# Kernel optimization log

Hardware: AMD Instinct MI355X
Metric: run time of the kernel (lower is better)

The kernel has to match this reference:

```python
import jax, jax.numpy as jnp
import numpy as np

N = 50000          # nodes per side (variables == clauses here)
IN, HID, OUT = 64, 128, 128
H = 4              # attention heads (self and cross)
P = 2              # num_meta_paths
E = 640000         # edges per graph
NEG = 0.2          # leaky_relu negative slope


def _glorot(key, shape):
    fan = shape[-2] + shape[-1]
    return (jax.random.normal(key, shape) * jnp.sqrt(2.0 / fan)).astype(jnp.float32)


def _ln(x, g, b):
    mu = x.mean(-1, keepdims=True)
    v = ((x - mu) ** 2).mean(-1, keepdims=True)
    return (x - mu) / jnp.sqrt(v + 1e-5) * g + b


def _segment_softmax(s, seg, num):
    # s: [E, H]; softmax over edges sharing the same seg id
    smax = jax.ops.segment_max(s, seg, num_segments=num)
    e = jnp.exp(s - smax[seg])
    den = jax.ops.segment_sum(e, seg, num_segments=num)
    return e / (den[seg] + 1e-16)


def _agg(alpha, feats, src, dst, num):
    # out[d, h, c] = sum_{e: dst[e]=d} alpha[e,h] * feats[src[e], c]
    gathered = feats[src]  # [E, C]
    outs = [jax.ops.segment_sum(alpha[:, h:h + 1] * gathered, dst, num_segments=num)
            for h in range(alpha.shape[1])]
    return jnp.stack(outs, axis=1)  # [num, H, C]


def _hga_self(x, adj, W, att_l, att_r, bias):
    # homogeneous HGAConv with self loops, concat=False (mean over heads)
    n = x.shape[0]
    xl = x @ W.T                      # [N, C]
    al = xl @ att_l                   # [N, H]
    ar = xl @ att_r                   # [N, H]
    loops = jnp.arange(n)
    src = jnp.concatenate([adj[0], loops])
    dst = jnp.concatenate([adj[1], loops])
    score = al[dst] + ar[src]         # edge_score: a_l[adj[1]] + a_r[adj[0]]
    alpha = _segment_softmax(jax.nn.leaky_relu(score, NEG), dst, n)
    out = _agg(alpha, xl, src, dst, n).mean(axis=1)  # [N, C]
    return out + bias


def _hga_cross(xv, xc, adj, Wl, Wr, att_l, att_r, bias):
    # bipartite HGAConv: adj[1] indexes var nodes, adj[0] indexes cls nodes
    n, m = xv.shape[0], xc.shape[0]
    xl = xv @ Wl.T
    xr = xc @ Wr.T
    al = xl @ att_l
    ar = xr @ att_r
    ar_ = xl @ att_r
    al_ = xr @ att_l
    c_idx, v_idx = adj[0], adj[1]
    score = al[v_idx] + ar[c_idx]        # -> normalized per var node
    score_ = ar_[v_idx] + al_[c_idx]     # transposed direction -> per cls node
    alpha = _segment_softmax(jax.nn.leaky_relu(score, NEG), v_idx, n)
    alpha_ = _segment_softmax(jax.nn.leaky_relu(score_, NEG), c_idx, m)
    out_var = _agg(alpha, xr, c_idx, v_idx, n).mean(axis=1) + bias   # [n, OUT]
    out_cls = _agg(alpha_, xl, v_idx, c_idx, m).mean(axis=1) + bias  # [m, OUT]
    return out_var, out_cls


def setup_inputs() -> dict:
    key = jax.random.key(0)
    ks = jax.random.split(key, 32)
    d = {}
    d['x_var'] = jax.random.normal(ks[0], (N, IN), dtype=jnp.float32)
    d['x_cls'] = jax.random.normal(ks[1], (N, IN), dtype=jnp.float32)
    d['mp_var'] = jax.random.randint(ks[2], (P, 2, E), 0, N)
    d['mp_cls'] = jax.random.randint(ks[3], (P, 2, E), 0, N)
    d['adj_pos'] = jax.random.randint(ks[4], (2, E), 0, N)
    d['adj_neg'] = jax.random.randint(ks[5], (2, E), 0, N)
    d['W_var_emb'] = _glorot(ks[6], (HID, IN))
    d['W_cls_emb'] = _glorot(ks[7], (HID, IN))
    d['ln_var_g'] = jnp.ones(HID); d['ln_var_b'] = jnp.zeros(HID)
    d['ln_cls_g'] = jnp.ones(HID); d['ln_cls_b'] = jnp.zeros(HID)
    d['var_pw'] = jnp.ones(P); d['cls_pw'] = jnp.ones(P)
    d['sv_W'] = _glorot(ks[8], (P, HID, HID))
    d['sv_al'] = _glorot(ks[9], (P, HID, H))
    d['sv_ar'] = _glorot(ks[10], (P, HID, H))
    d['sv_b'] = jnp.zeros((P, HID))
    d['sc_W'] = _glorot(ks[11], (P, HID, HID))
    d['sc_al'] = _glorot(ks[12], (P, HID, H))
    d['sc_ar'] = _glorot(ks[13], (P, HID, H))
    d['sc_b'] = jnp.zeros((P, HID))
    d['cp_Wl'] = _glorot(ks[14], (OUT, HID))
    d['cp_Wr'] = _glorot(ks[15], (OUT, HID))
    d['cp_al'] = _glorot(ks[16], (OUT, H))
    d['cp_ar'] = _glorot(ks[17], (OUT, H))
    d['cp_b'] = jnp.zeros(OUT)
    d['cn_Wl'] = _glorot(ks[18], (OUT, HID))
    d['cn_Wr'] = _glorot(ks[19], (OUT, HID))
    d['cn_al'] = _glorot(ks[20], (OUT, H))
    d['cn_ar'] = _glorot(ks[21], (OUT, H))
    d['cn_b'] = jnp.zeros(OUT)
    return d


def reference(x_var, x_cls, mp_var, mp_cls, adj_pos, adj_neg,
              W_var_emb, W_cls_emb, ln_var_g, ln_var_b, ln_cls_g, ln_cls_b,
              var_pw, cls_pw, sv_W, sv_al, sv_ar, sv_b, sc_W, sc_al, sc_ar, sc_b,
              cp_Wl, cp_Wr, cp_al, cp_ar, cp_b, cn_Wl, cn_Wr, cn_al, cn_ar, cn_b):
    xv = x_var @ W_var_emb.T          # [N, HID]
    xc = x_cls @ W_cls_emb.T
    # pre-norm residual self-attention, weighted sum over meta paths
    hv = _ln(xv, ln_var_g, ln_var_b)
    hc = _ln(xc, ln_cls_g, ln_cls_b)
    av = sum(var_pw[p] * _hga_self(hv, mp_var[p], sv_W[p], sv_al[p], sv_ar[p], sv_b[p]) for p in range(P))
    ac = sum(cls_pw[p] * _hga_self(hc, mp_cls[p], sc_W[p], sc_al[p], sc_ar[p], sc_b[p]) for p in range(P))
    xv = xv + av
    xc = xc + ac
    # bipartite cross attention over positive / negative literal edges
    vpos, cpos = _hga_cross(xv, xc, adj_pos, cp_Wl, cp_Wr, cp_al, cp_ar, cp_b)
    vneg, cneg = _hga_cross(xv, xc, adj_neg, cn_Wl, cn_Wr, cn_al, cn_ar, cn_b)
    return jnp.stack([vpos + vneg, cpos + cneg])  # [2, N, OUT]
```

## Files before the change

kernel.cpp:

```cpp
#include <hip/hip_runtime.h>
#include <hip/hip_bf16.h>

#define NN 50000
#define EE 640000
#define NEG 0.2f
#define CAP 64

#define BSH 9
#define NBKT 98
#define FCAP 7168
#define CHUNKA 8192
#define PA_B 79

struct Ptr8 { const int* p[8]; };
struct MArgs { const float* w[8]; const float* al[8]; const float* ar[8]; };

struct SegArg {
    const int* starts;
    const int* counts;
    const unsigned short* srt;
    const float* adst;
    const float* asrc;
    const unsigned short* feats;
    const float* pw;
    int pwi;
    int hasLoop;
};

struct ProjArgs {
    const float* in;
    const unsigned short* Wp0; const unsigned short* Wp1;
    const float* M0; const float* M1;
    unsigned short* ob0; unsigned short* ob1;
    float4* dl0; float4* dr0; float4* dl1; float4* dr1;
};

struct EmbArgs {
    const float* x; const float* Wt; const float* g; const float* b;
    const float* pw; const float* sb; float* F; float* C;
};

typedef __attribute__((ext_vector_type(8))) short short8;
typedef __attribute__((ext_vector_type(8))) unsigned short ushort8;
typedef __attribute__((ext_vector_type(4))) float floatx4;

__device__ __forceinline__ unsigned short f2bf(float x) {
    unsigned b = __float_as_uint(x);
    b = b + 0x7fffu + ((b >> 16) & 1u);
    return (unsigned short)(b >> 16);
}

__device__ __forceinline__ float4 leakyexp4(float4 ad, float4 as) {
    float v0 = ad.x + as.x, v1 = ad.y + as.y, v2 = ad.z + as.z, v3 = ad.w + as.w;
    v0 = v0 > 0.f ? v0 : NEG * v0;
    v1 = v1 > 0.f ? v1 : NEG * v1;
    v2 = v2 > 0.f ? v2 : NEG * v2;
    v3 = v3 > 0.f ? v3 : NEG * v3;
    return make_float4(__expf(v0), __expf(v1), __expf(v2), __expf(v3));
}

__global__ void prep_all(const float* __restrict__ wev, const float* __restrict__ wec,
                         float* __restrict__ Wt, MArgs a, float* __restrict__ Mbuf,
                         unsigned short* __restrict__ Wbf)
{
    int b = blockIdx.x;
    if (b < 64) {
        int i = b * 256 + threadIdx.x;
        if (i < 8192) { Wt[i] = wev[(i & 127) * 64 + (i >> 7)]; }
        else { int j = i - 8192; Wt[i] = wec[(j & 127) * 64 + (j >> 7)]; }
        return;
    }
    if (b < 128) {
        int tid = (b - 64) * 256 + threadIdx.x;
        int w = tid >> 11;
        int idx = tid & 2047;
        int tile = idx >> 6;
        int lane = idx & 63;
        int ct = tile >> 2, kc = tile & 3;
        int n = ct * 16 + (lane & 15);
        int k0 = kc * 32 + (lane >> 4) * 8;
        const float* src = a.w[w] + n * 128 + k0;
        short8 v;
#pragma unroll
        for (int j = 0; j < 8; j++) v[j] = (short)f2bf(src[j]);
        *(short8*)&Wbf[(size_t)tid * 8] = v;
        return;
    }
    {
        int w = b - 128;
        const float* W  = a.w[w];
        const float* AL = a.al[w];
        const float* AR = a.ar[w];
        for (int e = threadIdx.x; e < 1024; e += 256) {
            int k = e >> 3, h = e & 7;
            const float* att = (h < 4) ? AL : AR;
            int hh = h & 3;
            float s = 0.f;
            for (int c = 0; c < 128; c++) s += W[c * 128 + k] * att[c * 4 + hh];
            Mbuf[w * 1024 + e] = s;
        }
    }
}

__global__ void embed_ln2(EmbArgs Ea, EmbArgs Eb, int nb)
{
    __shared__ float lx[8][64];
    __shared__ float red[2][8][2];
    int half = blockIdx.x >= nb;
    const EmbArgs E = half ? Eb : Ea;
    int blk = blockIdx.x - (half ? nb : 0);
    int c = threadIdx.x;
    int n0 = blk * 8;
    for (int t = c; t < 8 * 64; t += 128) {
        lx[t >> 6][t & 63] = E.x[(size_t)(n0 + (t >> 6)) * 64 + (t & 63)];
    }
    __syncthreads();
    float acc[8];
#pragma unroll
    for (int m = 0; m < 8; m++) acc[m] = 0.f;
    for (int k = 0; k < 64; k++) {
        float w = E.Wt[k * 128 + c];
#pragma unroll
        for (int m = 0; m < 8; m++) acc[m] += lx[m][k] * w;
    }
    int lane = c & 63, wv = c >> 6;
#pragma unroll
    for (int m = 0; m < 8; m++) {
        float s1 = acc[m], s2 = acc[m] * acc[m];
        for (int off = 32; off; off >>= 1) { s1 += __shfl_xor(s1, off); s2 += __shfl_xor(s2, off); }
        if (lane == 0) { red[wv][m][0] = s1; red[wv][m][1] = s2; }
    }
    __syncthreads();
    float biassum = E.pw[0] * E.sb[c] + E.pw[1] * E.sb[128 + c];
    float gg = E.g[c], bb = E.b[c];
#pragma unroll
    for (int m = 0; m < 8; m++) {
        float s1 = red[0][m][0] + red[1][m][0];
        float s2 = red[0][m][1] + red[1][m][1];
        float mu  = s1 * (1.f / 128.f);
        float var = s2 * (1.f / 128.f) - mu * mu;
        float inv = rsqrtf(var + 1e-5f);
        float v = acc[m];
        size_t idx = (size_t)(n0 + m) * 128 + c;
        E.F[idx] = v + biassum;
        E.C[idx] = (v - mu) * inv * gg + bb;
    }
}

__global__ __launch_bounds__(256) void mfma_proj2(ProjArgs Pa, ProjArgs Pb, int nb)
{
    __shared__ float ML[2048];

    int half = blockIdx.x >= nb;
    const ProjArgs P = half ? Pb : Pa;
    int blk = blockIdx.x - (half ? nb : 0);

    int t = threadIdx.x;
    for (int i = t; i < 2048; i += 256) ML[i] = (i < 1024) ? P.M0[i] : P.M1[i - 1024];
    __syncthreads();

    int w = t >> 6, lane = t & 63;
    int rg = w & 1, chh = w >> 1;
    int ln = lane & 15, quad = lane >> 4;
    int rbase = blk * 32 + rg * 16;
    int row = rbase + ln;
    int arow = (row < NN) ? row : (NN - 1);
    const float* MLh = &ML[chh * 1024];

    short8 afrag[4];
    float p[8];
#pragma unroll
    for (int h = 0; h < 8; h++) p[h] = 0.f;
#pragma unroll
    for (int kc = 0; kc < 4; kc++) {
        int k0 = kc * 32 + quad * 8;
        const float* ap = P.in + (size_t)arow * 128 + k0;
        float av[8];
#pragma unroll
        for (int j = 0; j < 8; j++) av[j] = ap[j];
#pragma unroll
        for (int j = 0; j < 8; j++) {
            afrag[kc][j] = (short)f2bf(av[j]);
            const float* mrow = &MLh[(k0 + j) * 8];
#pragma unroll
            for (int h = 0; h < 8; h++) p[h] += av[j] * mrow[h];
        }
    }
#pragma unroll
    for (int h = 0; h < 8; h++) {
        p[h] += __shfl_xor(p[h], 16);
        p[h] += __shfl_xor(p[h], 32);
    }
    if (quad == 0 && row < NN) {
        if (chh == 0) {
            P.dl0[row] = make_float4(p[0], p[1], p[2], p[3]);
            P.dr0[row] = make_float4(p[4], p[5], p[6], p[7]);
        } else {
            P.dl1[row] = make_float4(p[0], p[1], p[2], p[3]);
            P.dr1[row] = make_float4(p[4], p[5], p[6], p[7]);
        }
    }

#pragma unroll
    for (int cti = 0; cti < 4; cti++) {
        int ct = chh * 4 + cti;
        floatx4 acc = {0.f, 0.f, 0.f, 0.f};
#pragma unroll
        for (int kc = 0; kc < 4; kc++) {
            short8 bfr = *(const short8*)&P.Wp0[(size_t)((ct * 4 + kc) * 64 + lane) * 8];
            acc = __builtin_amdgcn_mfma_f32_16x16x32_bf16(afrag[kc], bfr, acc, 0, 0, 0);
        }
#pragma unroll
        for (int r = 0; r < 4; r++) {
            int rr = rbase + quad * 4 + r;
            if (rr < NN) P.ob0[(size_t)rr * 128 + ct * 16 + ln] = f2bf(acc[r]);
        }
    }
#pragma unroll
    for (int cti = 0; cti < 4; cti++) {
        int ct = chh * 4 + cti;
        floatx4 acc = {0.f, 0.f, 0.f, 0.f};
#pragma unroll
        for (int kc = 0; kc < 4; kc++) {
            short8 bfr = *(const short8*)&P.Wp1[(size_t)((ct * 4 + kc) * 64 + lane) * 8];
            acc = __builtin_amdgcn_mfma_f32_16x16x32_bf16(afrag[kc], bfr, acc, 0, 0, 0);
        }
#pragma unroll
        for (int r = 0; r < 4; r++) {
            int rr = rbase + quad * 4 + r;
            if (rr < NN) P.ob1[(size_t)rr * 128 + ct * 16 + ln] = f2bf(acc[r]);
        }
    }
}

__global__ void bucket_count(Ptr8 dst, int* __restrict__ bcnt)
{
    __shared__ int h[NBKT];
    int l = blockIdx.x / PA_B, cb = blockIdx.x % PA_B;
    const int* dp = dst.p[l];
    for (int i = threadIdx.x; i < NBKT; i += 256) h[i] = 0;
    __syncthreads();
    int e0 = cb * CHUNKA;
    for (int i = threadIdx.x; i < CHUNKA; i += 256) {
        int e = e0 + i;
        if (e < EE) atomicAdd(&h[dp[e] >> BSH], 1);
    }
    __syncthreads();
    for (int i = threadIdx.x; i < NBKT; i += 256)
        if (h[i]) atomicAdd(&bcnt[l * NBKT + i], h[i]);
}

__global__ void bucket_scan(const int* __restrict__ bcnt, int* __restrict__ bstart,
                            int* __restrict__ bcur)
{
    __shared__ int sh[NBKT];
    int l = blockIdx.x;
    for (int i = threadIdx.x; i < NBKT; i += 256) sh[i] = bcnt[l * NBKT + i];
    __syncthreads();
    if (threadIdx.x == 0) {
        int acc = 0;
        for (int i = 0; i < NBKT; i++) { int t = sh[i]; sh[i] = acc; acc += t; }
    }
    __syncthreads();
    for (int i = threadIdx.x; i < NBKT; i += 256) {
        bstart[l * (NBKT + 1) + i] = sh[i];
        bcur[l * NBKT + i] = sh[i];
    }
    if (threadIdx.x == 0) bstart[l * (NBKT + 1) + NBKT] = EE;
}

__global__ void bucket_place(Ptr8 src, Ptr8 dst, int* __restrict__ bcur,
                             unsigned* __restrict__ recs)
{
    __shared__ int h[NBKT];
    __shared__ int base[NBKT];
    int l = blockIdx.x / PA_B, cb = blockIdx.x % PA_B;
    const int* sp = src.p[l];
    const int* dp = dst.p[l];
    for (int i = threadIdx.x; i < NBKT; i += 256) h[i] = 0;
    __syncthreads();
    int e0 = cb * CHUNKA;
    for (int i = threadIdx.x; i < CHUNKA; i += 256) {
        int e = e0 + i;
        if (e < EE) atomicAdd(&h[dp[e] >> BSH], 1);
    }
    __syncthreads();
    for (int i = threadIdx.x; i < NBKT; i += 256) {
        int c = h[i];
        base[i] = c ? atomicAdd(&bcur[l * NBKT + i], c) : 0;
        h[i] = 0;
    }
    __syncthreads();
    unsigned* rl = recs + (size_t)l * EE;
    for (int i = threadIdx.x; i < CHUNKA; i += 256) {
        int e = e0 + i;
        if (e >= EE) continue;
        int d = dp[e];
        int b = d >> BSH;
        int pos = base[b] + atomicAdd(&h[b], 1);
        rl[pos] = ((unsigned)sp[e] << 16) | (unsigned)d;
    }
}

__global__ __launch_bounds__(256) void bucket_final(
    const unsigned* __restrict__ recs, const int* __restrict__ bstart,
    int* __restrict__ starts8, int* __restrict__ counts8,
    unsigned short* __restrict__ sortedU)
{
    __shared__ unsigned R[FCAP];
    __shared__ int cnt[512];
    __shared__ int cur[512];
    __shared__ int psum[256];
    int l = blockIdx.x / NBKT, b = blockIdx.x % NBKT;
    int d0 = b << BSH;
    int nd = min(512, NN - d0);
    int ebase = bstart[l * (NBKT + 1) + b];
    int ecnt  = bstart[l * (NBKT + 1) + b + 1] - ebase;
    const unsigned* rp = recs + (size_t)l * EE + ebase;
    int t = threadIdx.x;
    bool inLds = (ecnt <= FCAP);

    for (int i = t; i < 512; i += 256) cnt[i] = 0;
    __syncthreads();
    for (int i = t; i < ecnt; i += 256) {
        unsigned r = rp[i];
        if (inLds) R[i] = r;
        atomicAdd(&cnt[(r & 0xffffu) - d0], 1);
    }
    __syncthreads();
    int s0 = cnt[2 * t] + cnt[2 * t + 1];
    psum[t] = s0;
    __syncthreads();
    for (int off = 1; off < 256; off <<= 1) {
        int x = (t >= off) ? psum[t - off] : 0;
        __syncthreads();
        psum[t] += x;
        __syncthreads();
    }
    int excl = psum[t] - s0;
    cur[2 * t] = excl;
    cur[2 * t + 1] = excl + cnt[2 * t];
    __syncthreads();
    for (int i = t; i < nd; i += 256) {
        starts8[l * NN + d0 + i] = ebase + cur[i];
        counts8[l * NN + d0 + i] = cnt[i];
    }
    __syncthreads();
    unsigned short* so = sortedU + (size_t)l * EE + ebase;
    for (int i = t; i < ecnt; i += 256) {
        unsigned r = inLds ? R[i] : rp[i];
        int dloc = (int)(r & 0xffffu) - d0;
        int pos = atomicAdd(&cur[dloc], 1);
        so[pos] = (unsigned short)(r >> 16);
    }
}

__global__ __launch_bounds__(256, 4) void agg_fused2(
    SegArg A0, SegArg B0, float* __restrict__ acc0,
    SegArg A1, SegArg B1, float* __restrict__ acc1,
    const float* __restrict__ bias0, const float* __restrict__ bias1,
    int nb, int mode)
{
    __shared__ float          wSh[16][CAP + 1];
    __shared__ unsigned short sSh[16][CAP + 2];

    int t = threadIdx.x;
    int gid = t >> 4, sub = t & 15;
    int seg = gid & 1;
    int half = blockIdx.x >= nb;
    int blk = blockIdx.x - (half ? nb : 0);
    int d = blk * 8 + (gid >> 1);

    const SegArg S = half ? (seg ? B1 : A1) : (seg ? B0 : A0);
    float* acc = half ? acc1 : acc0;

    int base = S.starts[d];
    int k = S.counts[d];
    int kTot = k + S.hasLoop;
    int kW = kTot < CAP ? kTot : CAP;

    float4 ad = *(const float4*)(S.adst + (size_t)d * 4);

    int ia = sub, ib = sub + 16, ic = sub + 32, id_ = sub + 48;
    int s0 = d, s1 = d, s2 = d, s3 = d;
    if (ia < kTot) { if (ia < k) s0 = (int)S.srt[base + ia]; sSh[gid][ia] = (unsigned short)s0; }
    if (ib < kTot) { if (ib < k) s1 = (int)S.srt[base + ib]; sSh[gid][ib] = (unsigned short)s1; }
    if (ic < kTot) { if (ic < k) s2 = (int)S.srt[base + ic]; sSh[gid][ic] = (unsigned short)s2; }
    if (id_ < kTot){ if (id_ < k) s3 = (int)S.srt[base + id_]; sSh[gid][id_] = (unsigned short)s3; }

    float4 as0 = {0,0,0,0}, as1 = {0,0,0,0}, as2 = {0,0,0,0}, as3 = {0,0,0,0};
    if (ia < kTot)  as0 = *(const float4*)(S.asrc + (size_t)s0 * 4);
    if (ib < kTot)  as1 = *(const float4*)(S.asrc + (size_t)s1 * 4);
    if (ic < kTot)  as2 = *(const float4*)(S.asrc + (size_t)s2 * 4);
    if (id_ < kTot) as3 = *(const float4*)(S.asrc + (size_t)s3 * 4);

    const unsigned short* fbase = S.feats + sub * 8;
    ushort8 pf0 = {0,0,0,0,0,0,0,0}, pf1 = pf0, pf2 = pf0, pf3 = pf0;
    if (0 < kW) { int q = sSh[gid][0]; pf0 = *(const ushort8*)(fbase + (size_t)q * 128); }
    if (1 < kW) { int q = sSh[gid][1]; pf1 = *(const ushort8*)(fbase + (size_t)q * 128); }
    if (2 < kW) { int q = sSh[gid][2]; pf2 = *(const ushort8*)(fbase + (size_t)q * 128); }
    if (3 < kW) { int q = sSh[gid][3]; pf3 = *(const ushort8*)(fbase + (size_t)q * 128); }

    float den0 = 0.f, den1 = 0.f, den2 = 0.f, den3 = 0.f;
    float4 e0 = {0,0,0,0}, e1 = {0,0,0,0}, e2 = {0,0,0,0}, e3 = {0,0,0,0};
    if (ia < kTot) { e0 = leakyexp4(ad, as0); den0 += e0.x; den1 += e0.y; den2 += e0.z; den3 += e0.w; }
    if (ib < kTot) { e1 = leakyexp4(ad, as1); den0 += e1.x; den1 += e1.y; den2 += e1.z; den3 += e1.w; }
    if (ic < kTot) { e2 = leakyexp4(ad, as2); den0 += e2.x; den1 += e2.y; den2 += e2.z; den3 += e2.w; }
    if (id_ < kTot){ e3 = leakyexp4(ad, as3); den0 += e3.x; den1 += e3.y; den2 += e3.z; den3 += e3.w; }
    for (int i = sub + 64; i < kTot; i += 16) {
        int s = (i < k) ? (int)S.srt[base + i] : d;
        float4 e = leakyexp4(ad, *(const float4*)(S.asrc + (size_t)s * 4));
        den0 += e.x; den1 += e.y; den2 += e.z; den3 += e.w;
    }
#pragma unroll
    for (int off = 1; off <= 8; off <<= 1) {
        den0 += __shfl_xor(den0, off); den1 += __shfl_xor(den1, off);
        den2 += __shfl_xor(den2, off); den3 += __shfl_xor(den3, off);
    }
    float scale = 0.25f * (S.pw ? S.pw[S.pwi] : 1.0f);
    float r0 = scale / (den0 + 1e-16f);
    float r1 = scale / (den1 + 1e-16f);
    float r2 = scale / (den2 + 1e-16f);
    float r3 = scale / (den3 + 1e-16f);

    if (ia < kTot)  wSh[gid][ia]  = e0.x * r0 + e0.y * r1 + e0.z * r2 + e0.w * r3;
    if (ib < kTot)  wSh[gid][ib]  = e1.x * r0 + e1.y * r1 + e1.z * r2 + e1.w * r3;
    if (ic < kTot)  wSh[gid][ic]  = e2.x * r0 + e2.y * r1 + e2.z * r2 + e2.w * r3;
    if (id_ < kTot) wSh[gid][id_] = e3.x * r0 + e3.y * r1 + e3.z * r2 + e3.w * r3;

    float a[8];
#pragma unroll
    for (int i = 0; i < 8; i++) a[i] = 0.f;
    if (0 < kW) { float w = wSh[gid][0];
#pragma unroll
        for (int i = 0; i < 8; i++) a[i] += w * __uint_as_float((unsigned)(unsigned short)pf0[i] << 16); }
    if (1 < kW) { float w = wSh[gid][1];
#pragma unroll
        for (int i = 0; i < 8; i++) a[i] += w * __uint_as_float((unsigned)(unsigned short)pf1[i] << 16); }
    if (2 < kW) { float w = wSh[gid][2];
#pragma unroll
        for (int i = 0; i < 8; i++) a[i] += w * __uint_as_float((unsigned)(unsigned short)pf2[i] << 16); }
    if (3 < kW) { float w = wSh[gid][3];
#pragma unroll
        for (int i = 0; i < 8; i++) a[i] += w * __uint_as_float((unsigned)(unsigned short)pf3[i] << 16); }

    int j = 4;
    for (; j + 4 <= kW; j += 4) {
        float w0 = wSh[gid][j],     w1 = wSh[gid][j + 1];
        float w2 = wSh[gid][j + 2], w3 = wSh[gid][j + 3];
        int t0 = sSh[gid][j],     t1 = sSh[gid][j + 1];
        int t2 = sSh[gid][j + 2], t3 = sSh[gid][j + 3];
        ushort8 va = *(const ushort8*)(fbase + (size_t)t0 * 128);
        ushort8 vb = *(const ushort8*)(fbase + (size_t)t1 * 128);
        ushort8 vc = *(const ushort8*)(fbase + (size_t)t2 * 128);
        ushort8 vd = *(const ushort8*)(fbase + (size_t)t3 * 128);
#pragma unroll
        for (int i = 0; i < 8; i++) {
            a[i] += w0 * __uint_as_float((unsigned)(unsigned short)va[i] << 16);
            a[i] += w1 * __uint_as_float((unsigned)(unsigned short)vb[i] << 16);
            a[i] += w2 * __uint_as_float((unsigned)(unsigned short)vc[i] << 16);
            a[i] += w3 * __uint_as_float((unsigned)(unsigned short)vd[i] << 16);
        }
    }
    for (; j < kW; ++j) {
        float w0 = wSh[gid][j];
        int t0 = sSh[gid][j];
        ushort8 v = *(const ushort8*)(fbase + (size_t)t0 * 128);
#pragma unroll
        for (int i = 0; i < 8; i++)
            a[i] += w0 * __uint_as_float((unsigned)(unsigned short)v[i] << 16);
    }
    for (int jj = CAP; jj < kTot; ++jj) {
        int s = (jj < k) ? (int)S.srt[base + jj] : d;
        float4 e = leakyexp4(ad, *(const float4*)(S.asrc + (size_t)s * 4));
        float wgt = e.x * r0 + e.y * r1 + e.z * r2 + e.w * r3;
        ushort8 v = *(const ushort8*)(fbase + (size_t)s * 128);
#pragma unroll
        for (int i = 0; i < 8; i++)
            a[i] += wgt * __uint_as_float((unsigned)(unsigned short)v[i] << 16);
    }

#pragma unroll
    for (int i = 0; i < 8; i++) a[i] += __shfl_xor(a[i], 16);

    if (seg == 0) {
        size_t idx = (size_t)d * 128 + sub * 8;
        float4* ap = (float4*)(acc + idx);
        float4 lo = make_float4(a[0], a[1], a[2], a[3]);
        float4 hi = make_float4(a[4], a[5], a[6], a[7]);
        if (mode) {
            const float4* b0 = (const float4*)(bias0 + sub * 8);
            const float4* b1 = (const float4*)(bias1 + sub * 8);
            float4 c0 = b0[0], c1 = b0[1], d0v = b1[0], d1v = b1[1];
            ap[0] = make_float4(c0.x + d0v.x + lo.x, c0.y + d0v.y + lo.y,
                                c0.z + d0v.z + lo.z, c0.w + d0v.w + lo.w);
            ap[1] = make_float4(c1.x + d1v.x + hi.x, c1.y + d1v.y + hi.y,
                                c1.z + d1v.z + hi.z, c1.w + d1v.w + hi.w);
        } else {
            float4 rr0 = ap[0], rr1 = ap[1];
            ap[0] = make_float4(rr0.x + lo.x, rr0.y + lo.y, rr0.z + lo.z, rr0.w + lo.w);
            ap[1] = make_float4(rr1.x + hi.x, rr1.y + hi.y, rr1.z + hi.z, rr1.w + hi.w);
        }
    }
}

extern "C" void kernel_launch(void* const* d_in, const int* in_sizes, int n_in,
                              void* d_out, int out_size, void* d_ws, size_t ws_size,
                              hipStream_t stream)
{
    const float* x_var   = (const float*)d_in[0];
    const float* x_cls   = (const float*)d_in[1];
    const int*   mp_var  = (const int*)d_in[2];
    const int*   mp_cls  = (const int*)d_in[3];
    const int*   adj_pos = (const int*)d_in[4];
    const int*   adj_neg = (const int*)d_in[5];
    const float* W_var_emb = (const float*)d_in[6];
    const float* W_cls_emb = (const float*)d_in[7];
    const float* ln_var_g = (const float*)d_in[8];
    const float* ln_var_b = (const float*)d_in[9];
    const float* ln_cls_g = (const float*)d_in[10];
    const float* ln_cls_b = (const float*)d_in[11];
    const float* var_pw = (const float*)d_in[12];
    const float* cls_pw = (const float*)d_in[13];
    const float* sv_W  = (const float*)d_in[14];
    const float* sv_al = (const float*)d_in[15];
    const float* sv_ar = (const float*)d_in[16];
    const float* sv_b  = (const float*)d_in[17];
    const float* sc_W  = (const float*)d_in[18];
    const float* sc_al = (const float*)d_in[19];
    const float* sc_ar = (const float*)d_in[20];
    const float* sc_b  = (const float*)d_in[21];
    const float* cp_Wl = (const float*)d_in[22];
    const float* cp_Wr = (const float*)d_in[23];
    const float* cp_al = (const float*)d_in[24];
    const float* cp_ar = (const float*)d_in[25];
    const float* cp_b  = (const float*)d_in[26];
    const float* cn_Wl = (const float*)d_in[27];
    const float* cn_Wr = (const float*)d_in[28];
    const float* cn_al = (const float*)d_in[29];
    const float* cn_ar = (const float*)d_in[30];
    const float* cn_b  = (const float*)d_in[31];

    float* out0 = (float*)d_out;
    float* out1 = out0 + (size_t)NN * 128;

    float* ws = (float*)d_ws;
    size_t off = 0;
    auto alloc = [&](size_t n) { float* p = ws + off; off += n; return p; };
    float* Wt   = alloc(16384);
    float* Mbuf = alloc(8 * 1024);
    unsigned short* Wbf = (unsigned short*)alloc(8 * 8192);
    float* F   = alloc((size_t)NN * 128);
    float* G   = alloc((size_t)NN * 128);
    float* C   = alloc((size_t)NN * 128);
    float* D   = alloc((size_t)NN * 128);
    unsigned short* B1 = (unsigned short*)alloc((size_t)NN * 64);
    unsigned short* B2 = (unsigned short*)alloc((size_t)NN * 64);
    unsigned short* Pc = (unsigned short*)alloc((size_t)NN * 64);
    unsigned short* Pd = (unsigned short*)alloc((size_t)NN * 64);
    float* dl   = alloc(NN * 4);
    float* dr   = alloc(NN * 4);
    float* dl2  = alloc(NN * 4);
    float* dr2  = alloc(NN * 4);
    float* dl3  = alloc(NN * 4);
    float* dr3  = alloc(NN * 4);
    float* dl4  = alloc(NN * 4);
    float* dr4  = alloc(NN * 4);
    int* counts8 = (int*)alloc(8 * NN);
    int* starts8 = (int*)alloc(8 * NN);
    int* bcnt    = (int*)alloc(8 * NBKT);
    int* bstart  = (int*)alloc(8 * (NBKT + 1));
    int* bcur    = (int*)alloc(8 * NBKT);
    unsigned* recs = (unsigned*)alloc((size_t)8 * EE);
    unsigned short* sortedU = (unsigned short*)alloc((size_t)4 * EE);

    const float* WtEv = Wt;
    const float* WtEc = Wt + 8192;

    Ptr8 srcP, dstP;
    srcP.p[0] = mp_var;            dstP.p[0] = mp_var + EE;
    srcP.p[1] = mp_var + 2 * EE;   dstP.p[1] = mp_var + 3 * EE;
    srcP.p[2] = mp_cls;            dstP.p[2] = mp_cls + EE;
    srcP.p[3] = mp_cls + 2 * EE;   dstP.p[3] = mp_cls + 3 * EE;
    srcP.p[4] = adj_pos;           dstP.p[4] = adj_pos + EE;
    srcP.p[5] = adj_pos + EE;      dstP.p[5] = adj_pos;
    srcP.p[6] = adj_neg;           dstP.p[6] = adj_neg + EE;
    srcP.p[7] = adj_neg + EE;      dstP.p[7] = adj_neg;

    MArgs ma;
    ma.w[0] = sv_W;           ma.al[0] = sv_al;        ma.ar[0] = sv_ar;
    ma.w[1] = sv_W + 16384;   ma.al[1] = sv_al + 512;  ma.ar[1] = sv_ar + 512;
    ma.w[2] = sc_W;           ma.al[2] = sc_al;        ma.ar[2] = sc_ar;
    ma.w[3] = sc_W + 16384;   ma.al[3] = sc_al + 512;  ma.ar[3] = sc_ar + 512;
    ma.w[4] = cp_Wl;          ma.al[4] = cp_al;        ma.ar[4] = cp_ar;
    ma.w[5] = cp_Wr;          ma.al[5] = cp_al;        ma.ar[5] = cp_ar;
    ma.w[6] = cn_Wl;          ma.al[6] = cn_al;        ma.ar[6] = cn_ar;
    ma.w[7] = cn_Wr;          ma.al[7] = cn_al;        ma.ar[7] = cn_ar;

    hipMemsetAsync(bcnt, 0, 8 * NBKT * sizeof(int), stream);
    bucket_count<<<8 * PA_B, 256, 0, stream>>>(dstP, bcnt);
    bucket_scan<<<8, 256, 0, stream>>>(bcnt, bstart, bcur);
    bucket_place<<<8 * PA_B, 256, 0, stream>>>(srcP, dstP, bcur, recs);
    bucket_final<<<8 * NBKT, 256, 0, stream>>>(recs, bstart, starts8, counts8, sortedU);

    prep_all<<<136, 256, 0, stream>>>(W_var_emb, W_cls_emb, Wt, ma, Mbuf, Wbf);

    EmbArgs Ev = { x_var, WtEv, ln_var_g, ln_var_b, var_pw, sv_b, F, C };
    EmbArgs Ec = { x_cls, WtEc, ln_cls_g, ln_cls_b, cls_pw, sc_b, G, D };
    embed_ln2<<<2 * (NN / 8), 128, 0, stream>>>(Ev, Ec, NN / 8);

    const int PB = (NN + 31) / 32;
    const int AB = NN / 8;

    ProjArgs Ps0 = { C, Wbf + 0 * 16384, Wbf + 1 * 16384, Mbuf + 0 * 1024, Mbuf + 1 * 1024,
                     B1, B2, (float4*)dl, (float4*)dr, (float4*)dl2, (float4*)dr2 };
    ProjArgs Ps1 = { D, Wbf + 2 * 16384, Wbf + 3 * 16384, Mbuf + 2 * 1024, Mbuf + 3 * 1024,
                     Pc, Pd, (float4*)dl3, (float4*)dr3, (float4*)dl4, (float4*)dr4 };
    mfma_proj2<<<2 * PB, 256, 0, stream>>>(Ps0, Ps1, PB);

    {
        SegArg VA, VB, CA, CB;
        VA.starts = starts8 + 0 * NN; VA.counts = counts8 + 0 * NN;
        VA.srt = sortedU + (size_t)0 * EE;
        VA.adst = dl;  VA.asrc = dr;  VA.feats = B1; VA.pw = var_pw; VA.pwi = 0; VA.hasLoop = 1;
        VB.starts = starts8 + 1 * NN; VB.counts = counts8 + 1 * NN;
        VB.srt = sortedU + (size_t)1 * EE;
        VB.adst = dl2; VB.asrc = dr2; VB.feats = B2; VB.pw = var_pw; VB.pwi = 1; VB.hasLoop = 1;
        CA.starts = starts8 + 2 * NN; CA.counts = counts8 + 2 * NN;
        CA.srt = sortedU + (size_t)2 * EE;
        CA.adst = dl3; CA.asrc = dr3; CA.feats = Pc; CA.pw = cls_pw; CA.pwi = 0; CA.hasLoop = 1;
        CB.starts = starts8 + 3 * NN; CB.counts = counts8 + 3 * NN;
        CB.srt = sortedU + (size_t)3 * EE;
        CB.adst = dl4; CB.asrc = dr4; CB.feats = Pd; CB.pw = cls_pw; CB.pwi = 1; CB.hasLoop = 1;
        agg_fused2<<<2 * AB, 256, 0, stream>>>(VA, VB, F, CA, CB, G, cp_b, cn_b, AB, 0);
    }

    ProjArgs Pc0 = { F, Wbf + 4 * 16384, Wbf + 6 * 16384, Mbuf + 4 * 1024, Mbuf + 6 * 1024,
                     B1, Pc, (float4*)dl, (float4*)dr, (float4*)dl3, (float4*)dr3 };
    ProjArgs Pc1 = { G, Wbf + 5 * 16384, Wbf + 7 * 16384, Mbuf + 5 * 1024, Mbuf + 7 * 1024,
                     B2, Pd, (float4*)dl2, (float4*)dr2, (float4*)dl4, (float4*)dr4 };
    mfma_proj2<<<2 * PB, 256, 0, stream>>>(Pc0, Pc1, PB);

    {
        SegArg OA, OB, PA, PBs;
        OA.starts = starts8 + 4 * NN; OA.counts = counts8 + 4 * NN;
        OA.srt = sortedU + (size_t)4 * EE;
        OA.adst = dl;  OA.asrc = dr2; OA.feats = B2; OA.pw = nullptr; OA.pwi = 0; OA.hasLoop = 0;
        OB.starts = starts8 + 6 * NN; OB.counts = counts8 + 6 * NN;
        OB.srt = sortedU + (size_t)6 * EE;
        OB.adst = dl3; OB.asrc = dr4; OB.feats = Pd; OB.pw = nullptr; OB.pwi = 0; OB.hasLoop = 0;
        PA.starts = starts8 + 5 * NN; PA.counts = counts8 + 5 * NN;
        PA.srt = sortedU + (size_t)5 * EE;
        PA.adst = dl2; PA.asrc = dr;  PA.feats = B1; PA.pw = nullptr; PA.pwi = 0; PA.hasLoop = 0;
        PBs.starts = starts8 + 7 * NN; PBs.counts = counts8 + 7 * NN;
        PBs.srt = sortedU + (size_t)7 * EE;
        PBs.adst = dl4; PBs.asrc = dr3; PBs.feats = Pc; PBs.pw = nullptr; PBs.pwi = 0; PBs.hasLoop = 0;
        agg_fused2<<<2 * AB, 256, 0, stream>>>(OA, OB, out0, PA, PBs, out1, cp_b, cn_b, AB, 1);
    }
}
```

Measured before the change: 652.1 us.

## Co-launch bucket sort phases with embedding and projection kernels

Merges the bucket-count pass into the embedding/LayerNorm kernel and the bucket-place pass into the MFMA projection kernel through block-index dispatch in a shared launch. The graph-sort launches now run alongside the dense work, so independent work overlaps and there are fewer launches. The embedding kernel also moves to 256-thread blocks that each handle 16 nodes. The cost is a larger shared-memory footprint per block and mixed block types inside one grid, which can hurt occupancy or balance.

Result: slower. 723.3 us (+10.9%).

```diff
diff --git a/kernel.cpp b/kernel.cpp
--- a/kernel.cpp
+++ b/kernel.cpp
@@ -102,18 +102,16 @@
     }
 }
 
-__global__ void embed_ln2(EmbArgs Ea, EmbArgs Eb, int nb)
-{
-    __shared__ float lx[8][64];
-    __shared__ float red[2][8][2];
-    int half = blockIdx.x >= nb;
-    const EmbArgs E = half ? Eb : Ea;
-    int blk = blockIdx.x - (half ? nb : 0);
-    int c = threadIdx.x;
-    int n0 = blk * 8;
-    for (int t = c; t < 8 * 64; t += 128) {
-        lx[t >> 6][t & 63] = E.x[(size_t)(n0 + (t >> 6)) * 64 + (t & 63)];
-    }
+
+__device__ __forceinline__ void embed_body16(const EmbArgs& E, int blk, char* smem)
+{
+    float (*lx)[8][64]  = (float(*)[8][64])smem;
+    float (*red)[2][8][2] = (float(*)[2][8][2])(smem + 4096);
+    int t = threadIdx.x;
+    int subh = t >> 7, c = t & 127;
+    int n0 = blk * 16 + subh * 8;
+    for (int tt = c; tt < 8 * 64; tt += 128)
+        lx[subh][tt >> 6][tt & 63] = E.x[(size_t)(n0 + (tt >> 6)) * 64 + (tt & 63)];
     __syncthreads();
     float acc[8];
 #pragma unroll
@@ -121,22 +119,22 @@
     for (int k = 0; k < 64; k++) {
         float w = E.Wt[k * 128 + c];
 #pragma unroll
-        for (int m = 0; m < 8; m++) acc[m] += lx[m][k] * w;
+        for (int m = 0; m < 8; m++) acc[m] += lx[subh][m][k] * w;
     }
     int lane = c & 63, wv = c >> 6;
 #pragma unroll
     for (int m = 0; m < 8; m++) {
         float s1 = acc[m], s2 = acc[m] * acc[m];
         for (int off = 32; off; off >>= 1) { s1 += __shfl_xor(s1, off); s2 += __shfl_xor(s2, off); }
-        if (lane == 0) { red[wv][m][0] = s1; red[wv][m][1] = s2; }
+        if (lane == 0) { red[subh][wv][m][0] = s1; red[subh][wv][m][1] = s2; }
     }
     __syncthreads();
     float biassum = E.pw[0] * E.sb[c] + E.pw[1] * E.sb[128 + c];
     float gg = E.g[c], bb = E.b[c];
 #pragma unroll
     for (int m = 0; m < 8; m++) {
-        float s1 = red[0][m][0] + red[1][m][0];
-        float s2 = red[0][m][1] + red[1][m][1];
+        float s1 = red[subh][0][m][0] + red[subh][1][m][0];
+        float s2 = red[subh][0][m][1] + red[subh][1][m][1];
         float mu  = s1 * (1.f / 128.f);
         float var = s2 * (1.f / 128.f) - mu * mu;
         float inv = rsqrtf(var + 1e-5f);
@@ -147,96 +145,11 @@
     }
 }
 
-__global__ __launch_bounds__(256) void mfma_proj2(ProjArgs Pa, ProjArgs Pb, int nb)
-{
-    __shared__ float ML[2048];
-
-    int half = blockIdx.x >= nb;
-    const ProjArgs P = half ? Pb : Pa;
-    int blk = blockIdx.x - (half ? nb : 0);
-
-    int t = threadIdx.x;
-    for (int i = t; i < 2048; i += 256) ML[i] = (i < 1024) ? P.M0[i] : P.M1[i - 1024];
-    __syncthreads();
-
-    int w = t >> 6, lane = t & 63;
-    int rg = w & 1, chh = w >> 1;
-    int ln = lane & 15, quad = lane >> 4;
-    int rbase = blk * 32 + rg * 16;
-    int row = rbase + ln;
-    int arow = (row < NN) ? row : (NN - 1);
-    const float* MLh = &ML[chh * 1024];
-
-    short8 afrag[4];
-    float p[8];
-#pragma unroll
-    for (int h = 0; h < 8; h++) p[h] = 0.f;
-#pragma unroll
-    for (int kc = 0; kc < 4; kc++) {
-        int k0 = kc * 32 + quad * 8;
-        const float* ap = P.in + (size_t)arow * 128 + k0;
-        float av[8];
-#pragma unroll
-        for (int j = 0; j < 8; j++) av[j] = ap[j];
-#pragma unroll
-        for (int j = 0; j < 8; j++) {
-            afrag[kc][j] = (short)f2bf(av[j]);
-            const float* mrow = &MLh[(k0 + j) * 8];
-#pragma unroll
-            for (int h = 0; h < 8; h++) p[h] += av[j] * mrow[h];
-        }
-    }
-#pragma unroll
-    for (int h = 0; h < 8; h++) {
-        p[h] += __shfl_xor(p[h], 16);
-        p[h] += __shfl_xor(p[h], 32);
-    }
-    if (quad == 0 && row < NN) {
-        if (chh == 0) {
-            P.dl0[row] = make_float4(p[0], p[1], p[2], p[3]);
-            P.dr0[row] = make_float4(p[4], p[5], p[6], p[7]);
-        } else {
-            P.dl1[row] = make_float4(p[0], p[1], p[2], p[3]);
-            P.dr1[row] = make_float4(p[4], p[5], p[6], p[7]);
-        }
-    }
-
-#pragma unroll
-    for (int cti = 0; cti < 4; cti++) {
-        int ct = chh * 4 + cti;
-        floatx4 acc = {0.f, 0.f, 0.f, 0.f};
-#pragma unroll
-        for (int kc = 0; kc < 4; kc++) {
-            short8 bfr = *(const short8*)&P.Wp0[(size_t)((ct * 4 + kc) * 64 + lane) * 8];
-            acc = __builtin_amdgcn_mfma_f32_16x16x32_bf16(afrag[kc], bfr, acc, 0, 0, 0);
-        }
-#pragma unroll
-        for (int r = 0; r < 4; r++) {
-            int rr = rbase + quad * 4 + r;
-            if (rr < NN) P.ob0[(size_t)rr * 128 + ct * 16 + ln] = f2bf(acc[r]);
-        }
-    }
-#pragma unroll
-    for (int cti = 0; cti < 4; cti++) {
-        int ct = chh * 4 + cti;
-        floatx4 acc = {0.f, 0.f, 0.f, 0.f};
-#pragma unroll
-        for (int kc = 0; kc < 4; kc++) {
-            short8 bfr = *(const short8*)&P.Wp1[(size_t)((ct * 4 + kc) * 64 + lane) * 8];
-            acc = __builtin_amdgcn_mfma_f32_16x16x32_bf16(afrag[kc], bfr, acc, 0, 0, 0);
-        }
-#pragma unroll
-        for (int r = 0; r < 4; r++) {
-            int rr = rbase + quad * 4 + r;
-            if (rr < NN) P.ob1[(size_t)rr * 128 + ct * 16 + ln] = f2bf(acc[r]);
-        }
-    }
-}
-
-__global__ void bucket_count(Ptr8 dst, int* __restrict__ bcnt)
-{
-    __shared__ int h[NBKT];
-    int l = blockIdx.x / PA_B, cb = blockIdx.x % PA_B;
+__device__ __forceinline__ void count_body(const Ptr8& dst, int idx, int* __restrict__ bcnt,
+                                           char* smem)
+{
+    int* h = (int*)smem;
+    int l = idx / PA_B, cb = idx % PA_B;
     const int* dp = dst.p[l];
     for (int i = threadIdx.x; i < NBKT; i += 256) h[i] = 0;
     __syncthreads();
@@ -250,31 +163,13 @@
         if (h[i]) atomicAdd(&bcnt[l * NBKT + i], h[i]);
 }
 
-__global__ void bucket_scan(const int* __restrict__ bcnt, int* __restrict__ bstart,
-                            int* __restrict__ bcur)
-{
-    __shared__ int sh[NBKT];
-    int l = blockIdx.x;
-    for (int i = threadIdx.x; i < NBKT; i += 256) sh[i] = bcnt[l * NBKT + i];
-    __syncthreads();
-    if (threadIdx.x == 0) {
-        int acc = 0;
-        for (int i = 0; i < NBKT; i++) { int t = sh[i]; sh[i] = acc; acc += t; }
-    }
-    __syncthreads();
-    for (int i = threadIdx.x; i < NBKT; i += 256) {
-        bstart[l * (NBKT + 1) + i] = sh[i];
-        bcur[l * NBKT + i] = sh[i];
-    }
-    if (threadIdx.x == 0) bstart[l * (NBKT + 1) + NBKT] = EE;
-}
-
-__global__ void bucket_place(Ptr8 src, Ptr8 dst, int* __restrict__ bcur,
-                             unsigned* __restrict__ recs)
-{
-    __shared__ int h[NBKT];
-    __shared__ int base[NBKT];
-    int l = blockIdx.x / PA_B, cb = blockIdx.x % PA_B;
+__device__ __forceinline__ void place_body(const Ptr8& src, const Ptr8& dst, int idx,
+                                           int* __restrict__ bcur, unsigned* __restrict__ recs,
+                                           char* smem)
+{
+    int* h = (int*)smem;
+    int* base = h + 128;
+    int l = idx / PA_B, cb = idx % PA_B;
     const int* sp = src.p[l];
     const int* dp = dst.p[l];
     for (int i = threadIdx.x; i < NBKT; i += 256) h[i] = 0;
@@ -300,6 +195,139 @@
         int pos = base[b] + atomicAdd(&h[b], 1);
         rl[pos] = ((unsigned)sp[e] << 16) | (unsigned)d;
     }
+}
+
+__device__ __forceinline__ void proj_body(const ProjArgs& P, int blk, float* ML)
+{
+    int t = threadIdx.x;
+    for (int i = t; i < 2048; i += 256) ML[i] = (i < 1024) ? P.M0[i] : P.M1[i - 1024];
+    __syncthreads();
+
+    int w = t >> 6, lane = t & 63;
+    int rg = w & 1, chh = w >> 1;
+    int ln = lane & 15, quad = lane >> 4;
+    int rbase = blk * 32 + rg * 16;
+    int row = rbase + ln;
+    int arow = (row < NN) ? row : (NN - 1);
+    const float* MLh = &ML[chh * 1024];
+
+    short8 afrag[4];
+    float p[8];
+#pragma unroll
+    for (int h = 0; h < 8; h++) p[h] = 0.f;
+#pragma unroll
+    for (int kc = 0; kc < 4; kc++) {
+        int k0 = kc * 32 + quad * 8;
+        const float* ap = P.in + (size_t)arow * 128 + k0;
+        float av[8];
+#pragma unroll
+        for (int j = 0; j < 8; j++) av[j] = ap[j];
+#pragma unroll
+        for (int j = 0; j < 8; j++) {
+            afrag[kc][j] = (short)f2bf(av[j]);
+            const float* mrow = &MLh[(k0 + j) * 8];
+#pragma unroll
+            for (int h = 0; h < 8; h++) p[h] += av[j] * mrow[h];
+        }
+    }
+#pragma unroll
+    for (int h = 0; h < 8; h++) {
+        p[h] += __shfl_xor(p[h], 16);
+        p[h] += __shfl_xor(p[h], 32);
+    }
+    if (quad == 0 && row < NN) {
+        if (chh == 0) {
+            P.dl0[row] = make_float4(p[0], p[1], p[2], p[3]);
+            P.dr0[row] = make_float4(p[4], p[5], p[6], p[7]);
+        } else {
+            P.dl1[row] = make_float4(p[0], p[1], p[2], p[3]);
+            P.dr1[row] = make_float4(p[4], p[5], p[6], p[7]);
+        }
+    }
+
+#pragma unroll
+    for (int cti = 0; cti < 4; cti++) {
+        int ct = chh * 4 + cti;
+        floatx4 acc = {0.f, 0.f, 0.f, 0.f};
+#pragma unroll
+        for (int kc = 0; kc < 4; kc++) {
+            short8 bfr = *(const short8*)&P.Wp0[(size_t)((ct * 4 + kc) * 64 + lane) * 8];
+            acc = __builtin_amdgcn_mfma_f32_16x16x32_bf16(afrag[kc], bfr, acc, 0, 0, 0);
+        }
+#pragma unroll
+        for (int r = 0; r < 4; r++) {
+            int rr = rbase + quad * 4 + r;
+            if (rr < NN) P.ob0[(size_t)rr * 128 + ct * 16 + ln] = f2bf(acc[r]);
+        }
+    }
+#pragma unroll
+    for (int cti = 0; cti < 4; cti++) {
+        int ct = chh * 4 + cti;
+        floatx4 acc = {0.f, 0.f, 0.f, 0.f};
+#pragma unroll
+        for (int kc = 0; kc < 4; kc++) {
+            short8 bfr = *(const short8*)&P.Wp1[(size_t)((ct * 4 + kc) * 64 + lane) * 8];
+            acc = __builtin_amdgcn_mfma_f32_16x16x32_bf16(afrag[kc], bfr, acc, 0, 0, 0);
+        }
+#pragma unroll
+        for (int r = 0; r < 4; r++) {
+            int rr = rbase + quad * 4 + r;
+            if (rr < NN) P.ob1[(size_t)rr * 128 + ct * 16 + ln] = f2bf(acc[r]);
+        }
+    }
+}
+
+__global__ __launch_bounds__(256) void fused_embed_count(
+    EmbArgs Ea, EmbArgs Eb, int nbE, Ptr8 dst, int* __restrict__ bcnt)
+{
+    __shared__ __align__(16) char smem[4608];
+    int b = blockIdx.x;
+    if (b < 2 * nbE) {
+        int side = b >= nbE;
+        embed_body16(side ? Eb : Ea, b - (side ? nbE : 0), smem);
+    } else {
+        count_body(dst, b - 2 * nbE, bcnt, smem);
+    }
+}
+
+__global__ __launch_bounds__(256) void fused_proj_place(
+    ProjArgs Pa, ProjArgs Pb, int nbP,
+    Ptr8 src, Ptr8 dst, int* __restrict__ bcur, unsigned* __restrict__ recs)
+{
+    __shared__ __align__(16) char smem[8448];
+    int b = blockIdx.x;
+    if (b < 2 * nbP) {
+        int half = b >= nbP;
+        proj_body(half ? Pb : Pa, b - (half ? nbP : 0), (float*)smem);
+    } else {
+        place_body(src, dst, b - 2 * nbP, bcur, recs, smem);
+    }
+}
+
+__global__ __launch_bounds__(256) void mfma_proj2(ProjArgs Pa, ProjArgs Pb, int nb)
+{
+    __shared__ __align__(16) float ML[2112];
+    int half = blockIdx.x >= nb;
+    proj_body(half ? Pb : Pa, blockIdx.x - (half ? nb : 0), ML);
+}
+
+__global__ void bucket_scan(const int* __restrict__ bcnt, int* __restrict__ bstart,
+                            int* __restrict__ bcur)
+{
+    __shared__ int sh[NBKT];
+    int l = blockIdx.x;
+    for (int i = threadIdx.x; i < NBKT; i += 256) sh[i] = bcnt[l * NBKT + i];
+    __syncthreads();
+    if (threadIdx.x == 0) {
+        int acc = 0;
+        for (int i = 0; i < NBKT; i++) { int t = sh[i]; sh[i] = acc; acc += t; }
+    }
+    __syncthreads();
+    for (int i = threadIdx.x; i < NBKT; i += 256) {
+        bstart[l * (NBKT + 1) + i] = sh[i];
+        bcur[l * NBKT + i] = sh[i];
+    }
+    if (threadIdx.x == 0) bstart[l * (NBKT + 1) + NBKT] = EE;
 }
 
 __global__ __launch_bounds__(256) void bucket_final(
@@ -597,26 +625,27 @@
     ma.w[6] = cn_Wl;          ma.al[6] = cn_al;        ma.ar[6] = cn_ar;
     ma.w[7] = cn_Wr;          ma.al[7] = cn_al;        ma.ar[7] = cn_ar;
 
+    const int PB = (NN + 31) / 32;
+    const int AB = NN / 8;
+    const int NBE = NN / 16;
+
     hipMemsetAsync(bcnt, 0, 8 * NBKT * sizeof(int), stream);
-    bucket_count<<<8 * PA_B, 256, 0, stream>>>(dstP, bcnt);
-    bucket_scan<<<8, 256, 0, stream>>>(bcnt, bstart, bcur);
-    bucket_place<<<8 * PA_B, 256, 0, stream>>>(srcP, dstP, bcur, recs);
-    bucket_final<<<8 * NBKT, 256, 0, stream>>>(recs, bstart, starts8, counts8, sortedU);
-
     prep_all<<<136, 256, 0, stream>>>(W_var_emb, W_cls_emb, Wt, ma, Mbuf, Wbf);
 
     EmbArgs Ev = { x_var, WtEv, ln_var_g, ln_var_b, var_pw, sv_b, F, C };
     EmbArgs Ec = { x_cls, WtEc, ln_cls_g, ln_cls_b, cls_pw, sc_b, G, D };
-    embed_ln2<<<2 * (NN / 8), 128, 0, stream>>>(Ev, Ec, NN / 8);
-
-    const int PB = (NN + 31) / 32;
-    const int AB = NN / 8;
+    fused_embed_count<<<2 * NBE + 8 * PA_B, 256, 0, stream>>>(Ev, Ec, NBE, dstP, bcnt);
+
+    bucket_scan<<<8, 256, 0, stream>>>(bcnt, bstart, bcur);
 
     ProjArgs Ps0 = { C, Wbf + 0 * 16384, Wbf + 1 * 16384, Mbuf + 0 * 1024, Mbuf + 1 * 1024,
                      B1, B2, (float4*)dl, (float4*)dr, (float4*)dl2, (float4*)dr2 };
     ProjArgs Ps1 = { D, Wbf + 2 * 16384, Wbf + 3 * 16384, Mbuf + 2 * 1024, Mbuf + 3 * 1024,
                      Pc, Pd, (float4*)dl3, (float4*)dr3, (float4*)dl4, (float4*)dr4 };
-    mfma_proj2<<<2 * PB, 256, 0, stream>>>(Ps0, Ps1, PB);
+    fused_proj_place<<<2 * PB + 8 * PA_B, 256, 0, stream>>>(Ps0, Ps1, PB,
+                                                            srcP, dstP, bcur, recs);
+
+    bucket_final<<<8 * NBKT, 256, 0, stream>>>(recs, bstart, starts8, counts8, sortedU);
 
     {
         SegArg VA, VB, CA, CB;
```
